# Performance work log

Measured on AMD Instinct MI355X. Metric: run time of the kernel, lower is better.

## Reference

```python
import jax, jax.numpy as jnp
import numpy as np
import math

D_MODEL = 1024
NHEAD = 16
MAX_SUP = 4
DK = D_MODEL // NHEAD
DM = D_MODEL * MAX_SUP  # 4096
B, S = 2, 1024


def setup_inputs() -> dict:
    key = jax.random.key(0)
    ks = jax.random.split(key, 12)
    std = 0.02
    inp = {
        'q': jax.random.normal(ks[0], (B, S, DM), jnp.float32),
        'k': jax.random.normal(ks[1], (B, S, DM), jnp.float32),
        'v': jax.random.normal(ks[2], (B, S, DM), jnp.float32),
        'Wq': jax.random.normal(ks[3], (DM, DM), jnp.float32) * std,
        'bq': jnp.zeros((DM,), jnp.float32),
        'Wk': jax.random.normal(ks[4], (DM, DM), jnp.float32) * std,
        'bk': jnp.zeros((DM,), jnp.float32),
        'Wv': jax.random.normal(ks[5], (DM, DM), jnp.float32) * std,
        'bv': jnp.zeros((DM,), jnp.float32),
        'interference': jax.random.normal(ks[6], (NHEAD, MAX_SUP, MAX_SUP), jnp.float32),
        'amp': jnp.ones((1,), jnp.float32),
        'Wo': jax.random.normal(ks[7], (DM, DM), jnp.float32) * std,
        'bo': jnp.zeros((DM,), jnp.float32),
    }
    return inp


def reference(q, k, v, Wq, bq, Wk, bk, Wv, bv, interference, amp, Wo, bo):
    # forward_superposition path (is_superposition=True, no masks, eval dropout)
    b, s, dm = q.shape
    H, M = interference.shape[0], interference.shape[1]
    dk = dm // (H * M)

    def proj(x, W, bias):
        y = x @ W.T + bias                      # [b, s, dm] torch nn.Linear
        y = y.reshape(b, s, H, dk, M)           # view(B,S,H,d_k,M)
        return jnp.transpose(y, (0, 2, 1, 3, 4))  # [b, H, s, dk, M]

    qh = proj(q, Wq, bq)
    kh = proj(k, Wk, bk)
    vh = proj(v, Wv, bv)

    def interfere(x):
        # per-head einsum 'bsdi,ij->bsdj' vectorized over heads
        return x + 0.1 * amp[0] * jnp.einsum('bhsdi,hij->bhsdj', x, interference)

    qh, kh, vh = interfere(qh), interfere(kh), interfere(vh)

    # attention per superposition dim, vectorized over m
    scores = jnp.einsum('bhqdm,bhkdm->bhqkm', qh, kh) / math.sqrt(dk)
    weights = jax.nn.softmax(scores, axis=3)    # softmax over keys
    out = jnp.einsum('bhqkm,bhkdm->bhqdm', weights, vh)

    out = jnp.transpose(out, (0, 2, 1, 3, 4)).reshape(b, s, dm)  # permute(0,2,1,3,4)
    return out @ Wo.T + bo
```

## Files before the change

kernel.cpp:

```cpp
#include <hip/hip_runtime.h>
#include <hip/hip_bf16.h>

typedef unsigned short u16;
typedef unsigned int u32;
typedef __attribute__((ext_vector_type(8))) short bf16x8;
typedef __attribute__((ext_vector_type(4))) float f32x4;

__device__ __forceinline__ u16 f2bf(float f) {
    u32 u = __float_as_uint(f);
    u += 0x7FFFu + ((u >> 16) & 1u);
    return (u16)(u >> 16);
}
__device__ __forceinline__ u32 pack2(float a, float b) {
    return (u32)f2bf(a) | ((u32)f2bf(b) << 16);
}

#define GLDS16(gp, lp)                                                          \
    __builtin_amdgcn_global_load_lds(                                           \
        (const __attribute__((address_space(1))) void*)(gp),                    \
        (__attribute__((address_space(3))) void*)(lp), 16, 0, 0)

__global__ __launch_bounds__(256) void cast_f32_bf16(const float* __restrict__ src,
                                                     u16* __restrict__ dst, int n8) {
    int stride = gridDim.x * blockDim.x;
    for (int i = blockIdx.x * blockDim.x + threadIdx.x; i < n8; i += stride) {
        const float4* sp = (const float4*)src + (size_t)i * 2;
        float4 a = sp[0], b = sp[1];
        uint4 o;
        o.x = pack2(a.x, a.y);
        o.y = pack2(a.z, a.w);
        o.z = pack2(b.x, b.y);
        o.w = pack2(b.z, b.w);
        ((uint4*)dst)[i] = o;
    }
}

template <bool PROJ>
__global__ __launch_bounds__(256) void gemm_bt(
    const u16* __restrict__ Ab, const u16* __restrict__ Bb,
    const float* __restrict__ b0, const float* __restrict__ b1, const float* __restrict__ b2,
    const float* __restrict__ interf, const float* __restrict__ amp,
    u16* __restrict__ Yb, float* __restrict__ Cf) {
    constexpr int M = 2048, N = 4096, K = 4096;
    const int tid = threadIdx.x;
    const int l = tid & 63, w = tid >> 6;
    const int z = PROJ ? blockIdx.z : 0;
    const int n0 = blockIdx.x * 128, m0 = blockIdx.y * 128;
    const u16* A = Ab + (size_t)z * M * K;
    const u16* B = Bb + (size_t)z * N * K;

    __shared__ u16 As[128 * 64];
    __shared__ u16 Bs[128 * 64];
    __shared__ float Ish[256];
    if (PROJ) Ish[tid] = interf[tid];

    const int wr = (w >> 1) * 64, wc = (w & 1) * 64;
    const int fr = l & 15, fg = l >> 4;

    f32x4 acc[4][4] = {};

    int srow[4], scol[4], soff[4];
    #pragma unroll
    for (int r = 0; r < 4; ++r) {
        int e = (r * 4 + w) * 512 + l * 8;
        soff[r] = e;
        srow[r] = e >> 6;
        scol[r] = e & 63;
    }

    for (int kt = 0; kt < K; kt += 64) {
        #pragma unroll
        for (int r = 0; r < 4; ++r) {
            GLDS16(A + (size_t)(m0 + srow[r]) * K + kt + scol[r], As + soff[r]);
            GLDS16(B + (size_t)(n0 + srow[r]) * K + kt + scol[r], Bs + soff[r]);
        }
        __syncthreads();
        #pragma unroll
        for (int kb = 0; kb < 2; ++kb) {
            bf16x8 af[4], bfr[4];
            #pragma unroll
            for (int mi = 0; mi < 4; ++mi)
                af[mi] = *(const bf16x8*)&As[(wr + mi * 16 + fr) * 64 + kb * 32 + fg * 8];
            #pragma unroll
            for (int nj = 0; nj < 4; ++nj)
                bfr[nj] = *(const bf16x8*)&Bs[(wc + nj * 16 + fr) * 64 + kb * 32 + fg * 8];
            #pragma unroll
            for (int mi = 0; mi < 4; ++mi)
                #pragma unroll
                for (int nj = 0; nj < 4; ++nj)
                    acc[mi][nj] = __builtin_amdgcn_mfma_f32_16x16x32_bf16(af[mi], bfr[nj],
                                                                          acc[mi][nj], 0, 0, 0);
        }
        __syncthreads();
    }

    if (PROJ) {
        const float camp = 0.1f * amp[0];
        const float* bias = (z == 0) ? b0 : (z == 1) ? b1 : b2;
        const float qs = (z == 0) ? 0.125f : 1.0f;
        #pragma unroll
        for (int nj = 0; nj < 4; ++nj) {
            const int ncol = n0 + wc + nj * 16 + fr;
            const int h = ncol >> 8, m = ncol & 3;
            const float c0 = Ish[h * 16 + (m ^ 0) * 4 + m];
            const float c1 = Ish[h * 16 + (m ^ 1) * 4 + m];
            const float c2 = Ish[h * 16 + (m ^ 2) * 4 + m];
            const float c3 = Ish[h * 16 + (m ^ 3) * 4 + m];
            const float bn = bias[ncol];
            #pragma unroll
            for (int mi = 0; mi < 4; ++mi) {
                #pragma unroll
                for (int j = 0; j < 4; ++j) {
                    float y = acc[mi][nj][j] + bn;
                    float x1 = __shfl_xor(y, 1);
                    float x2 = __shfl_xor(y, 2);
                    float x3 = __shfl_xor(y, 3);
                    float s = y * c0 + x1 * c1 + x2 * c2 + x3 * c3;
                    float zv = (y + camp * s) * qs;
                    int mr = m0 + wr + mi * 16 + fg * 4 + j;
                    Yb[((size_t)z * M + mr) * N + ncol] = f2bf(zv);
                }
            }
        }
    } else {
        #pragma unroll
        for (int nj = 0; nj < 4; ++nj) {
            const int ncol = n0 + wc + nj * 16 + fr;
            const float bn = b0[ncol];
            #pragma unroll
            for (int mi = 0; mi < 4; ++mi) {
                #pragma unroll
                for (int j = 0; j < 4; ++j) {
                    int mr = m0 + wr + mi * 16 + fg * 4 + j;
                    Cf[(size_t)mr * N + ncol] = acc[mi][nj][j] + bn;
                }
            }
        }
    }
}

__global__ __launch_bounds__(256) void repack_fwd(const u16* __restrict__ Y, u16* __restrict__ Ai) {
    const int bid = blockIdx.x;
    const int st = bid & 15, h = (bid >> 4) & 15, b = (bid >> 8) & 1, p = bid >> 9;
    const int tid = threadIdx.x;
    __shared__ u16 T[64][264];
    const int s0 = st * 64;
    {
        const int sr = tid >> 2, q4 = tid & 3;
        const u16* src = Y + ((size_t)p * 2048 + b * 1024 + s0 + sr) * 4096 + h * 256 + q4 * 64;
        #pragma unroll
        for (int ji = 0; ji < 8; ++ji)
            *(uint4*)&T[sr][q4 * 64 + ji * 8] = *(const uint4*)(src + ji * 8);
    }
    __syncthreads();
    {
        const int s = tid & 63, wv = tid >> 6;
        #pragma unroll
        for (int m = 0; m < 4; ++m) {
            u16* dst = Ai + ((size_t)p * 128 + ((b * 16 + h) * 4 + m)) * 65536 + (size_t)(s0 + s) * 64;
            #pragma unroll
            for (int db = 0; db < 2; ++db) {
                int d0 = wv * 16 + db * 8;
                uint4 o;
                o.x = (u32)T[s][(d0 + 0) * 4 + m] | ((u32)T[s][(d0 + 1) * 4 + m] << 16);
                o.y = (u32)T[s][(d0 + 2) * 4 + m] | ((u32)T[s][(d0 + 3) * 4 + m] << 16);
                o.z = (u32)T[s][(d0 + 4) * 4 + m] | ((u32)T[s][(d0 + 5) * 4 + m] << 16);
                o.w = (u32)T[s][(d0 + 6) * 4 + m] | ((u32)T[s][(d0 + 7) * 4 + m] << 16);
                *(uint4*)(dst + d0) = o;
            }
        }
    }
}

__global__ __launch_bounds__(256) void repack_back(const u16* __restrict__ Ao, u16* __restrict__ An) {
    const int bid = blockIdx.x;
    const int st = bid & 15, h = (bid >> 4) & 15, b = bid >> 8;
    const int tid = threadIdx.x;
    __shared__ u16 T[64][264];
    const int s0 = st * 64;
    {
        const int sr = tid >> 2, q4 = tid & 3;
        #pragma unroll
        for (int m = 0; m < 4; ++m) {
            const u16* src = Ao + (size_t)((b * 16 + h) * 4 + m) * 65536 + (size_t)(s0 + sr) * 64 + q4 * 16;
            #pragma unroll
            for (int db = 0; db < 2; ++db) {
                uint4 vv = *(const uint4*)(src + db * 8);
                const u16* pv = (const u16*)&vv;
                #pragma unroll
                for (int j = 0; j < 8; ++j)
                    T[sr][(q4 * 16 + db * 8 + j) * 4 + m] = pv[j];
            }
        }
    }
    __syncthreads();
    {
        const int sr = tid >> 2, q4 = tid & 3;
        u16* dst = An + (size_t)(b * 1024 + s0 + sr) * 4096 + h * 256 + q4 * 64;
        #pragma unroll
        for (int ji = 0; ji < 8; ++ji)
            *(uint4*)(dst + ji * 8) = *(const uint4*)&T[sr][q4 * 64 + ji * 8];
    }
}

__global__ __launch_bounds__(256) void attn_fwd(const u16* __restrict__ Qa,
                                                const u16* __restrict__ Ka,
                                                const u16* __restrict__ Va,
                                                u16* __restrict__ Oa) {
    const int orig = blockIdx.x;
    const int wgid = (orig & 7) * 256 + (orig >> 3);
    const int p = wgid >> 4, qt = wgid & 15;
    const int tid = threadIdx.x, l = tid & 63, w = tid >> 6;
    const int fr = l & 15, fg = l >> 4;
    __shared__ u16 Qs[64][72];
    __shared__ u16 Ks[64][72];
    __shared__ u16 Vt[64][72];
    __shared__ u16 Ps[4][16][72];
    const size_t pb = (size_t)p * 65536;
    const int q0 = qt * 64;
    {
        const int r = tid >> 2, c = (tid & 3) * 16;
        const uint4* g = (const uint4*)(Qa + pb + (size_t)(q0 + r) * 64 + c);
        uint4 v0 = g[0], v1 = g[1];
        *(uint4*)&Qs[r][c] = v0;
        *(uint4*)&Qs[r][c + 8] = v1;
    }
    __syncthreads();
    bf16x8 aq0 = *(const bf16x8*)&Qs[w * 16 + fr][fg * 8];
    bf16x8 aq1 = *(const bf16x8*)&Qs[w * 16 + fr][32 + fg * 8];
    f32x4 oacc[4] = {};
    float mrow[4] = {-3.0e38f, -3.0e38f, -3.0e38f, -3.0e38f};
    float lrow[4] = {};
    const float L2E = 1.44269504088896f;

    for (int t = 0; t < 16; ++t) {
        const int k0 = t * 64;
        {
            const int r = tid >> 2, c = (tid & 3) * 16;
            const uint4* gk = (const uint4*)(Ka + pb + (size_t)(k0 + r) * 64 + c);
            uint4 ka = gk[0], kb2 = gk[1];
            *(uint4*)&Ks[r][c] = ka;
            *(uint4*)&Ks[r][c + 8] = kb2;
            const uint4* gv = (const uint4*)(Va + pb + (size_t)(k0 + r) * 64 + c);
            uint4 va = gv[0], vb = gv[1];
            const u16* pv0 = (const u16*)&va;
            const u16* pv1 = (const u16*)&vb;
            #pragma unroll
            for (int j = 0; j < 8; ++j) Vt[c + j][r] = pv0[j];
            #pragma unroll
            for (int j = 0; j < 8; ++j) Vt[c + 8 + j][r] = pv1[j];
        }
        __syncthreads();

        f32x4 sa[4] = {};
        __builtin_amdgcn_s_setprio(1);
        #pragma unroll
        for (int nj = 0; nj < 4; ++nj) {
            bf16x8 kf = *(const bf16x8*)&Ks[nj * 16 + fr][fg * 8];
            sa[nj] = __builtin_amdgcn_mfma_f32_16x16x32_bf16(aq0, kf, sa[nj], 0, 0, 0);
        }
        #pragma unroll
        for (int nj = 0; nj < 4; ++nj) {
            bf16x8 kf = *(const bf16x8*)&Ks[nj * 16 + fr][32 + fg * 8];
            sa[nj] = __builtin_amdgcn_mfma_f32_16x16x32_bf16(aq1, kf, sa[nj], 0, 0, 0);
        }
        __builtin_amdgcn_s_setprio(0);

        float tm[4], mn[4], scl[4], rs[4];
        #pragma unroll
        for (int j = 0; j < 4; ++j)
            tm[j] = fmaxf(fmaxf(sa[0][j], sa[1][j]), fmaxf(sa[2][j], sa[3][j]));
        #pragma unroll
        for (int off = 1; off < 16; off <<= 1)
            #pragma unroll
            for (int j = 0; j < 4; ++j) tm[j] = fmaxf(tm[j], __shfl_xor(tm[j], off));
        #pragma unroll
        for (int j = 0; j < 4; ++j) {
            mn[j] = fmaxf(mrow[j], tm[j]);
            scl[j] = exp2f((mrow[j] - mn[j]) * L2E);
            rs[j] = 0.0f;
        }
        #pragma unroll
        for (int nj = 0; nj < 4; ++nj) {
            #pragma unroll
            for (int j = 0; j < 4; ++j) {
                float pv = exp2f((sa[nj][j] - mn[j]) * L2E);
                rs[j] += pv;
                Ps[w][fg * 4 + j][nj * 16 + fr] = f2bf(pv);
            }
        }
        #pragma unroll
        for (int off = 1; off < 16; off <<= 1)
            #pragma unroll
            for (int j = 0; j < 4; ++j) rs[j] += __shfl_xor(rs[j], off);
        #pragma unroll
        for (int j = 0; j < 4; ++j) {
            lrow[j] = lrow[j] * scl[j] + rs[j];
            mrow[j] = mn[j];
        }
        #pragma unroll
        for (int nd = 0; nd < 4; ++nd)
            #pragma unroll
            for (int j = 0; j < 4; ++j) oacc[nd][j] *= scl[j];

        {
            bf16x8 pa0 = *(const bf16x8*)&Ps[w][fr][fg * 8];
            bf16x8 pa1 = *(const bf16x8*)&Ps[w][fr][32 + fg * 8];
            __builtin_amdgcn_s_setprio(1);
            #pragma unroll
            for (int nd = 0; nd < 4; ++nd) {
                bf16x8 vf = *(const bf16x8*)&Vt[nd * 16 + fr][fg * 8];
                oacc[nd] = __builtin_amdgcn_mfma_f32_16x16x32_bf16(pa0, vf, oacc[nd], 0, 0, 0);
            }
            #pragma unroll
            for (int nd = 0; nd < 4; ++nd) {
                bf16x8 vf = *(const bf16x8*)&Vt[nd * 16 + fr][32 + fg * 8];
                oacc[nd] = __builtin_amdgcn_mfma_f32_16x16x32_bf16(pa1, vf, oacc[nd], 0, 0, 0);
            }
            __builtin_amdgcn_s_setprio(0);
        }
        __syncthreads();
    }

    float inv[4];
    #pragma unroll
    for (int j = 0; j < 4; ++j) inv[j] = 1.0f / lrow[j];
    #pragma unroll
    for (int nd = 0; nd < 4; ++nd)
        #pragma unroll
        for (int j = 0; j < 4; ++j)
            Oa[pb + (size_t)(q0 + w * 16 + fg * 4 + j) * 64 + nd * 16 + fr] =
                f2bf(oacc[nd][j] * inv[j]);
}

extern "C" void kernel_launch(void* const* d_in, const int* in_sizes, int n_in,
                              void* d_out, int out_size, void* d_ws, size_t ws_size,
                              hipStream_t stream) {
    const float* q      = (const float*)d_in[0];
    const float* k      = (const float*)d_in[1];
    const float* v      = (const float*)d_in[2];
    const float* Wq     = (const float*)d_in[3];
    const float* bq     = (const float*)d_in[4];
    const float* Wk     = (const float*)d_in[5];
    const float* bk     = (const float*)d_in[6];
    const float* Wv     = (const float*)d_in[7];
    const float* bv     = (const float*)d_in[8];
    const float* interf = (const float*)d_in[9];
    const float* amp    = (const float*)d_in[10];
    const float* Wo     = (const float*)d_in[11];
    const float* bo     = (const float*)d_in[12];
    (void)in_sizes; (void)n_in; (void)out_size; (void)ws_size;

    char* ws = (char*)d_ws;
    u16* Wbf = (u16*)ws;
    u16* Xbf = (u16*)(ws + 100663296);
    u16* Ybf = (u16*)(ws + 150994944);
    u16* ATi = Xbf;
    u16* ATo = (u16*)(ws + 150994944);
    u16* ATn = (u16*)(ws + 167772160);

    const size_t WE = 16777216;
    const size_t XE = 8388608;

    cast_f32_bf16<<<2048, 256, 0, stream>>>(Wq, Wbf + 0 * WE, (int)(WE / 8));
    cast_f32_bf16<<<2048, 256, 0, stream>>>(Wk, Wbf + 1 * WE, (int)(WE / 8));
    cast_f32_bf16<<<2048, 256, 0, stream>>>(Wv, Wbf + 2 * WE, (int)(WE / 8));
    cast_f32_bf16<<<2048, 256, 0, stream>>>(q, Xbf + 0 * XE, (int)(XE / 8));
    cast_f32_bf16<<<2048, 256, 0, stream>>>(k, Xbf + 1 * XE, (int)(XE / 8));
    cast_f32_bf16<<<2048, 256, 0, stream>>>(v, Xbf + 2 * XE, (int)(XE / 8));

    gemm_bt<true><<<dim3(32, 16, 3), 256, 0, stream>>>(Xbf, Wbf, bq, bk, bv, interf, amp,
                                                       Ybf, nullptr);

    cast_f32_bf16<<<2048, 256, 0, stream>>>(Wo, Wbf + 0 * WE, (int)(WE / 8));

    repack_fwd<<<1536, 256, 0, stream>>>(Ybf, ATi);

    attn_fwd<<<dim3(2048), 256, 0, stream>>>(ATi, ATi + XE, ATi + 2 * XE, ATo);

    repack_back<<<512, 256, 0, stream>>>(ATo, ATn);

    gemm_bt<false><<<dim3(32, 16, 1), 256, 0, stream>>>(ATn, Wbf + 0 * WE, bo, nullptr, nullptr,
                                                        nullptr, nullptr, nullptr, (float*)d_out);
}
```

Baseline: 988.3 us.

## Use 256x256 8-wave pipelined GEMM with swizzled LDS for QKV projections

Replaces the QKV projection GEMM with a 512-thread kernel computing 256x256 output tiles. It stages A/B into double-buffered, XOR-swizzled LDS via global_load_lds in four quadrant phases, interleaving the next tile's loads with MFMA work using explicit waitcnt, barriers and setprio. The aim is to raise operand reuse, avoid LDS bank conflicts and overlap memory latency with compute in the dominant GEMM. The output GEMM is split into its own non-templated kernel, unchanged otherwise. The larger tile cuts the projection grid to 384 blocks, which may leave parts of the GPU underused, and the hand-written wait counts carry correctness risk.

```diff
diff --git a/kernel.cpp b/kernel.cpp
--- a/kernel.cpp
+++ b/kernel.cpp
@@ -19,6 +19,12 @@
     __builtin_amdgcn_global_load_lds(                                           \
         (const __attribute__((address_space(1))) void*)(gp),                    \
         (__attribute__((address_space(3))) void*)(lp), 16, 0, 0)
+
+#define FENCE asm volatile("" ::: "memory")
+#define BAR()  do { FENCE; __builtin_amdgcn_s_barrier(); FENCE; } while (0)
+#define VM2()  asm volatile("s_waitcnt vmcnt(2)" ::: "memory")
+#define LG0()  do { asm volatile("s_waitcnt lgkmcnt(0)" ::: "memory");          \
+                    __builtin_amdgcn_sched_barrier(0); } while (0)
 
 __global__ __launch_bounds__(256) void cast_f32_bf16(const float* __restrict__ src,
                                                      u16* __restrict__ dst, int n8) {
@@ -35,24 +41,185 @@
     }
 }
 
-template <bool PROJ>
-__global__ __launch_bounds__(256) void gemm_bt(
+__global__ __launch_bounds__(512, 1) void gemm8_proj(
     const u16* __restrict__ Ab, const u16* __restrict__ Bb,
     const float* __restrict__ b0, const float* __restrict__ b1, const float* __restrict__ b2,
     const float* __restrict__ interf, const float* __restrict__ amp,
-    u16* __restrict__ Yb, float* __restrict__ Cf) {
-    constexpr int M = 2048, N = 4096, K = 4096;
+    u16* __restrict__ Yb) {
+    constexpr int K = 4096, NT = 64;
+    __shared__ u16 As[2][16384];
+    __shared__ u16 Bs[2][16384];
+    __shared__ float Ish[256];
+    const int tid = threadIdx.x;
+    if (tid < 256) Ish[tid] = interf[tid];
+    const int l = tid & 63, w = tid >> 6;
+    const int wrow = w >> 2, wcol = w & 3;
+    const int fr = l & 15, fg = l >> 4;
+    const int z = blockIdx.z;
+    const int n0 = blockIdx.x * 256, m0 = blockIdx.y * 256;
+    const u16* A = Ab + (size_t)z * 2048 * K;
+    const u16* B = Bb + (size_t)z * 4096 * K;
+
+    const int lr = l >> 3;
+    const int sc = ((l & 7) ^ lr) * 8;
+    const size_t aBase = (size_t)(m0 + w * 8 + lr) * K + sc;
+    const size_t bBase = (size_t)(n0 + w * 8 + lr) * K + sc;
+    const int ldsLane = w * 512 + l * 8;
+
+#define STG_A(h, tt) do { int bsel_ = ((tt) & 1); int ts_ = (tt) < NT ? (tt) : NT - 1;        \
+    GLDS16(A + aBase + (size_t)((h) * 128) * K + ts_ * 64, &As[bsel_][(h) * 8192 + ldsLane]); \
+    GLDS16(A + aBase + (size_t)((h) * 128 + 64) * K + ts_ * 64,                               \
+           &As[bsel_][(h) * 8192 + 4096 + ldsLane]); } while (0)
+#define STG_B(h, tt) do { int bsel_ = ((tt) & 1); int ts_ = (tt) < NT ? (tt) : NT - 1;        \
+    GLDS16(B + bBase + (size_t)((h) * 128) * K + ts_ * 64, &Bs[bsel_][(h) * 8192 + ldsLane]); \
+    GLDS16(B + bBase + (size_t)((h) * 128 + 64) * K + ts_ * 64,                               \
+           &Bs[bsel_][(h) * 8192 + 4096 + ldsLane]); } while (0)
+
+    const int kx = (fr & 7) * 8;
+    const int ca = (fg * 8) ^ kx;
+    const int cb = (32 + fg * 8) ^ kx;
+    const int aR = (wrow * 64 + fr) * 64;
+    const int bR = (wcol * 32 + fr) * 64;
+
+    f32x4 acc[2][2][4][2] = {};
+    bf16x8 a[4][2], q0b[2][2], q1b[2][2];
+
+    STG_A(0, 0);
+    STG_B(0, 0);
+    STG_B(1, 0);
+    VM2();
+    BAR();
+
+    for (int t = 0; t < NT; ++t) {
+        const int bs = t & 1;
+        const u16* Ac = As[bs];
+        const u16* Bc = Bs[bs];
+        #pragma unroll
+        for (int mf = 0; mf < 4; ++mf) {
+            a[mf][0] = *(const bf16x8*)&Ac[aR + mf * 1024 + ca];
+            a[mf][1] = *(const bf16x8*)&Ac[aR + mf * 1024 + cb];
+        }
+        #pragma unroll
+        for (int nf = 0; nf < 2; ++nf) {
+            q0b[nf][0] = *(const bf16x8*)&Bc[bR + nf * 1024 + ca];
+            q0b[nf][1] = *(const bf16x8*)&Bc[bR + nf * 1024 + cb];
+        }
+        STG_A(1, t);
+        BAR();
+        LG0();
+        __builtin_amdgcn_s_setprio(1);
+        #pragma unroll
+        for (int mf = 0; mf < 4; ++mf)
+            #pragma unroll
+            for (int nf = 0; nf < 2; ++nf)
+                #pragma unroll
+                for (int kk = 0; kk < 2; ++kk)
+                    acc[0][0][mf][nf] = __builtin_amdgcn_mfma_f32_16x16x32_bf16(
+                        a[mf][kk], q0b[nf][kk], acc[0][0][mf][nf], 0, 0, 0);
+        __builtin_amdgcn_s_setprio(0);
+        VM2();
+        BAR();
+        #pragma unroll
+        for (int nf = 0; nf < 2; ++nf) {
+            q1b[nf][0] = *(const bf16x8*)&Bc[bR + 8192 + nf * 1024 + ca];
+            q1b[nf][1] = *(const bf16x8*)&Bc[bR + 8192 + nf * 1024 + cb];
+        }
+        STG_A(0, t + 1);
+        BAR();
+        LG0();
+        __builtin_amdgcn_s_setprio(1);
+        #pragma unroll
+        for (int mf = 0; mf < 4; ++mf)
+            #pragma unroll
+            for (int nf = 0; nf < 2; ++nf)
+                #pragma unroll
+                for (int kk = 0; kk < 2; ++kk)
+                    acc[0][1][mf][nf] = __builtin_amdgcn_mfma_f32_16x16x32_bf16(
+                        a[mf][kk], q1b[nf][kk], acc[0][1][mf][nf], 0, 0, 0);
+        __builtin_amdgcn_s_setprio(0);
+        VM2();
+        BAR();
+        #pragma unroll
+        for (int mf = 0; mf < 4; ++mf) {
+            a[mf][0] = *(const bf16x8*)&Ac[aR + 8192 + mf * 1024 + ca];
+            a[mf][1] = *(const bf16x8*)&Ac[aR + 8192 + mf * 1024 + cb];
+        }
+        STG_B(0, t + 1);
+        BAR();
+        LG0();
+        __builtin_amdgcn_s_setprio(1);
+        #pragma unroll
+        for (int mf = 0; mf < 4; ++mf)
+            #pragma unroll
+            for (int nf = 0; nf < 2; ++nf)
+                #pragma unroll
+                for (int kk = 0; kk < 2; ++kk)
+                    acc[1][1][mf][nf] = __builtin_amdgcn_mfma_f32_16x16x32_bf16(
+                        a[mf][kk], q1b[nf][kk], acc[1][1][mf][nf], 0, 0, 0);
+        __builtin_amdgcn_s_setprio(0);
+        BAR();
+        STG_B(1, t + 1);
+        BAR();
+        __builtin_amdgcn_s_setprio(1);
+        #pragma unroll
+        for (int mf = 0; mf < 4; ++mf)
+            #pragma unroll
+            for (int nf = 0; nf < 2; ++nf)
+                #pragma unroll
+                for (int kk = 0; kk < 2; ++kk)
+                    acc[1][0][mf][nf] = __builtin_amdgcn_mfma_f32_16x16x32_bf16(
+                        a[mf][kk], q0b[nf][kk], acc[1][0][mf][nf], 0, 0, 0);
+        __builtin_amdgcn_s_setprio(0);
+        VM2();
+        BAR();
+    }
+#undef STG_A
+#undef STG_B
+
+    const float camp = 0.1f * amp[0];
+    const float* bias = (z == 0) ? b0 : (z == 1) ? b1 : b2;
+    const float qs = (z == 0) ? 0.125f : 1.0f;
+    #pragma unroll
+    for (int qc = 0; qc < 2; ++qc)
+        #pragma unroll
+        for (int nf = 0; nf < 2; ++nf) {
+            const int ncol = n0 + qc * 128 + wcol * 32 + nf * 16 + fr;
+            const int hh = ncol >> 8, mm = fr & 3;
+            const float i0 = Ish[hh * 16 + (mm ^ 0) * 4 + mm];
+            const float i1 = Ish[hh * 16 + (mm ^ 1) * 4 + mm];
+            const float i2 = Ish[hh * 16 + (mm ^ 2) * 4 + mm];
+            const float i3 = Ish[hh * 16 + (mm ^ 3) * 4 + mm];
+            const float bn = bias[ncol];
+            #pragma unroll
+            for (int qr = 0; qr < 2; ++qr)
+                #pragma unroll
+                for (int mf = 0; mf < 4; ++mf)
+                    #pragma unroll
+                    for (int j = 0; j < 4; ++j) {
+                        float y = acc[qr][qc][mf][nf][j] + bn;
+                        float x1 = __shfl_xor(y, 1);
+                        float x2 = __shfl_xor(y, 2);
+                        float x3 = __shfl_xor(y, 3);
+                        float s = y * i0 + x1 * i1 + x2 * i2 + x3 * i3;
+                        float zv = (y + camp * s) * qs;
+                        int mr = m0 + qr * 128 + wrow * 64 + mf * 16 + fg * 4 + j;
+                        Yb[((size_t)z * 2048 + mr) * 4096 + ncol] = f2bf(zv);
+                    }
+        }
+}
+
+__global__ __launch_bounds__(256) void gemm_bt_f32(
+    const u16* __restrict__ Ab, const u16* __restrict__ Bb,
+    const float* __restrict__ b0, float* __restrict__ Cf) {
+    constexpr int K = 4096, N = 4096;
     const int tid = threadIdx.x;
     const int l = tid & 63, w = tid >> 6;
-    const int z = PROJ ? blockIdx.z : 0;
     const int n0 = blockIdx.x * 128, m0 = blockIdx.y * 128;
-    const u16* A = Ab + (size_t)z * M * K;
-    const u16* B = Bb + (size_t)z * N * K;
+    const u16* A = Ab;
+    const u16* B = Bb;
 
     __shared__ u16 As[128 * 64];
     __shared__ u16 Bs[128 * 64];
-    __shared__ float Ish[256];
-    if (PROJ) Ish[tid] = interf[tid];
 
     const int wr = (w >> 1) * 64, wc = (w & 1) * 64;
     const int fr = l & 15, fg = l >> 4;
@@ -94,46 +261,16 @@
         __syncthreads();
     }
 
-    if (PROJ) {
-        const float camp = 0.1f * amp[0];
-        const float* bias = (z == 0) ? b0 : (z == 1) ? b1 : b2;
-        const float qs = (z == 0) ? 0.125f : 1.0f;
-        #pragma unroll
-        for (int nj = 0; nj < 4; ++nj) {
-            const int ncol = n0 + wc + nj * 16 + fr;
-            const int h = ncol >> 8, m = ncol & 3;
-            const float c0 = Ish[h * 16 + (m ^ 0) * 4 + m];
-            const float c1 = Ish[h * 16 + (m ^ 1) * 4 + m];
-            const float c2 = Ish[h * 16 + (m ^ 2) * 4 + m];
-            const float c3 = Ish[h * 16 + (m ^ 3) * 4 + m];
-            const float bn = bias[ncol];
-            #pragma unroll
-            for (int mi = 0; mi < 4; ++mi) {
-                #pragma unroll
-                for (int j = 0; j < 4; ++j) {
-                    float y = acc[mi][nj][j] + bn;
-                    float x1 = __shfl_xor(y, 1);
-                    float x2 = __shfl_xor(y, 2);
-                    float x3 = __shfl_xor(y, 3);
-                    float s = y * c0 + x1 * c1 + x2 * c2 + x3 * c3;
-                    float zv = (y + camp * s) * qs;
-                    int mr = m0 + wr + mi * 16 + fg * 4 + j;
-                    Yb[((size_t)z * M + mr) * N + ncol] = f2bf(zv);
-                }
-            }
-        }
-    } else {
-        #pragma unroll
-        for (int nj = 0; nj < 4; ++nj) {
-            const int ncol = n0 + wc + nj * 16 + fr;
-            const float bn = b0[ncol];
-            #pragma unroll
-            for (int mi = 0; mi < 4; ++mi) {
-                #pragma unroll
-                for (int j = 0; j < 4; ++j) {
-                    int mr = m0 + wr + mi * 16 + fg * 4 + j;
-                    Cf[(size_t)mr * N + ncol] = acc[mi][nj][j] + bn;
-                }
+    #pragma unroll
+    for (int nj = 0; nj < 4; ++nj) {
+        const int ncol = n0 + wc + nj * 16 + fr;
+        const float bn = b0[ncol];
+        #pragma unroll
+        for (int mi = 0; mi < 4; ++mi) {
+            #pragma unroll
+            for (int j = 0; j < 4; ++j) {
+                int mr = m0 + wr + mi * 16 + fg * 4 + j;
+                Cf[(size_t)mr * N + ncol] = acc[mi][nj][j] + bn;
             }
         }
     }
@@ -369,8 +506,7 @@
     cast_f32_bf16<<<2048, 256, 0, stream>>>(k, Xbf + 1 * XE, (int)(XE / 8));
     cast_f32_bf16<<<2048, 256, 0, stream>>>(v, Xbf + 2 * XE, (int)(XE / 8));
 
-    gemm_bt<true><<<dim3(32, 16, 3), 256, 0, stream>>>(Xbf, Wbf, bq, bk, bv, interf, amp,
-                                                       Ybf, nullptr);
+    gemm8_proj<<<dim3(16, 8, 3), 512, 0, stream>>>(Xbf, Wbf, bq, bk, bv, interf, amp, Ybf);
 
     cast_f32_bf16<<<2048, 256, 0, stream>>>(Wo, Wbf + 0 * WE, (int)(WE / 8));
 
@@ -380,6 +516,5 @@
 
     repack_back<<<512, 256, 0, stream>>>(ATo, ATn);
 
-    gemm_bt<false><<<dim3(32, 16, 1), 256, 0, stream>>>(ATn, Wbf + 0 * WE, bo, nullptr, nullptr,
-                                                        nullptr, nullptr, nullptr, (float*)d_out);
-}
+    gemm_bt_f32<<<dim3(32, 16), 256, 0, stream>>>(ATn, Wbf + 0 * WE, bo, (float*)d_out);
+}
```

Measured after the change: 872.3 us. -11.7%, faster.
